# Kernel tuning notes

Hardware: AMD Instinct MI355X
Metric: run time of the kernel (lower is better)

The kernel has to match this reference:

```python
import jax, jax.numpy as jnp
import numpy as np

B, S, D, F, H = 32768, 3, 512, 512, 8
DH = F // H
NEG = 1e9


def setup_inputs() -> dict:
    key = jax.random.key(0)
    ks = jax.random.split(key, 13)
    mk = lambda i, shape: jax.random.normal(ks[i], shape, dtype=jnp.float32)
    return {
        "q": mk(0, (B, S, D)),
        "k": mk(1, (B, S, D)),
        "v": mk(2, (B, S, D)),
        "mask": jax.random.randint(ks[3], (B, S), 0, 2, dtype=jnp.int32),
        "Wq": mk(4, (D, F)) * 0.02, "bq": jnp.zeros((F,), jnp.float32),
        "Wk": mk(5, (D, F)) * 0.02, "bk": jnp.zeros((F,), jnp.float32),
        "Wv": mk(6, (D, F)) * 0.02, "bv": jnp.zeros((F,), jnp.float32),
        "Wo": mk(7, (F, F)) * 0.02, "bo": jnp.zeros((F,), jnp.float32),
    }


def _split_heads(x):
    # [B, S, F] -> [B, H, S, DH]
    b, s, _ = x.shape
    return x.reshape(b, s, H, DH).transpose(0, 2, 1, 3)


def reference(q, k, v, mask, Wq, bq, Wk, bk, Wv, bv, Wo, bo):
    qh = _split_heads(q @ Wq + bq)
    kh = _split_heads(k @ Wk + bk)
    vh = _split_heads(v @ Wv + bv)
    scores = jnp.einsum("bhqd,bhkd->bhqk", qh, kh) / np.sqrt(DH).astype(np.float32)
    m = mask.astype(scores.dtype) * NEG  # [B, S]
    scores = scores - m[:, None, None, :] - m[:, None, :, None]  # col + row mask
    w = jax.nn.softmax(scores, axis=-1)
    attn = jnp.einsum("bhqk,bhkd->bhqd", w, vh)  # [B, H, S, DH]
    attn = attn.transpose(0, 2, 1, 3).reshape(attn.shape[0], S, F)
    return attn @ Wo + bo
```

## Files before the change

### kernel.cpp

```cpp
#include <hip/hip_runtime.h>


typedef __bf16 bf16x8 __attribute__((ext_vector_type(8)));
typedef float f32x4 __attribute__((ext_vector_type(4)));

union U8 { bf16x8 v; unsigned short u[8]; unsigned int w[4]; uint4 q; };

__device__ __forceinline__ unsigned short f2bf(float f) {
  union { float f; unsigned int u; } v; v.f = f;
  unsigned int u = v.u;
  return (unsigned short)((u + 0x7FFFu + ((u >> 16) & 1u)) >> 16);
}
__device__ __forceinline__ unsigned int cvt_pk_bf16(float lo, float hi) {
  unsigned int r;
  asm volatile("v_cvt_pk_bf16_f32 %0, %1, %2" : "=v"(r) : "v"(lo), "v"(hi));
  return r;
}

__global__ void __launch_bounds__(256) wtrans(const float* __restrict__ W0,
                                              const float* __restrict__ W1,
                                              const float* __restrict__ W2,
                                              const float* __restrict__ W3,
                                              unsigned short* __restrict__ out) {
  __shared__ float tile[64][65];
  const float* W = (blockIdx.z == 0) ? W0 : (blockIdx.z == 1) ? W1
                   : (blockIdx.z == 2) ? W2 : W3;
  unsigned short* O = out + (size_t)blockIdx.z * 512 * 512;
  int t = threadIdx.x;
  int k0 = blockIdx.x * 64, n0 = blockIdx.y * 64;
#pragma unroll
  for (int i = 0; i < 4; ++i) {
    int r = (t >> 4) + i * 16;
    int c = (t & 15) * 4;
    float4 v = *(const float4*)(W + (k0 + r) * 512 + n0 + c);
    tile[r][c] = v.x; tile[r][c + 1] = v.y; tile[r][c + 2] = v.z; tile[r][c + 3] = v.w;
  }
  __syncthreads();
  int lane = t & 63, f = t >> 6;
  int lr = lane & 15, hi = lane >> 4;
#pragma unroll
  for (int i = 0; i < 2; ++i) {
    int g = f + i * 4;
    int n16l = g & 3, ksl = g >> 2;
    U8 pk;
#pragma unroll
    for (int e = 0; e < 8; ++e)
      pk.u[e] = f2bf(tile[ksl * 32 + hi * 8 + e][n16l * 16 + lr]);
    int n16 = (n0 >> 4) + n16l;
    int ksg = (k0 >> 5) + ksl;
    *(uint4*)(O + (((n16 * 16 + ksg) * 64 + lane) * 8)) = pk.q;
  }
}

#define SH_SCR  49152
#define SH_PS   65536
#define SH_MSK  71680
#define SH_BIAS 71872

__device__ __forceinline__ void stage48(const float* __restrict__ src, int row0,
                                        int t, char* smem) {
#pragma unroll 1
  for (int c = 0; c < 3; ++c) {
    float4 vals[4];
#pragma unroll
    for (int j = 0; j < 4; ++j) {
      int idx = t + (c * 4 + j) * 512;
      int row = idx >> 7, c4 = idx & 127;
      vals[j] = *(const float4*)(src + (size_t)(row0 + row) * 512 + c4 * 4);
    }
#pragma unroll
    for (int j = 0; j < 4; ++j) {
      int idx = t + (c * 4 + j) * 512;
      int row = idx >> 7, c4 = idx & 127;
      uint2 pk;
      pk.x = cvt_pk_bf16(vals[j].x, vals[j].y);
      pk.y = cvt_pk_bf16(vals[j].z, vals[j].w);
      *(uint2*)(smem + ((row * 1024 + c4 * 8) ^ ((row & 7) << 4))) = pk;
    }
  }
}

__device__ __forceinline__ void gemm_proj(const char* smem,
                                          const unsigned short* __restrict__ Bt,
                                          int w, int l, int lr, int lk8,
                                          f32x4 acc[3][4]) {
#pragma unroll 1
  for (int ks = 0; ks < 16; ++ks) {
    int kb = ks * 32 + lk8;
    bf16x8 a[3];
#pragma unroll
    for (int mt = 0; mt < 3; ++mt) {
      int row = mt * 16 + lr;
      a[mt] = *(const bf16x8*)(smem + ((row * 1024 + kb * 2) ^ ((row & 7) << 4)));
    }
#pragma unroll
    for (int np = 0; np < 2; ++np) {
      bf16x8 b[2];
#pragma unroll
      for (int j = 0; j < 2; ++j)
        b[j] = *(const bf16x8*)(Bt + (((w * 4 + np * 2 + j) * 16 + ks) * 64 + l) * 8);
#pragma unroll
      for (int j = 0; j < 2; ++j)
#pragma unroll
        for (int mt = 0; mt < 3; ++mt)
          acc[mt][np * 2 + j] =
              __builtin_amdgcn_mfma_f32_16x16x32_bf16(a[mt], b[j], acc[mt][np * 2 + j], 0, 0, 0);
    }
  }
}

__device__ __forceinline__ void tile_to_afrags(char* scr, const float* biasT, int bofs,
                                               const f32x4 acc[4], float scale,
                                               int lr, int hi, bf16x8* out) {
#pragma unroll
  for (int nt = 0; nt < 4; ++nt) {
    float bv = biasT[bofs + nt * 16];
#pragma unroll
    for (int r = 0; r < 4; ++r) {
      int row = 4 * hi + r;
      int col = nt * 16 + lr;
      int addr = (row * 128 + col * 2) ^ ((row & 7) << 4);
      *(unsigned short*)(scr + addr) = f2bf((acc[nt][r] + bv) * scale);
    }
  }
  asm volatile("s_waitcnt lgkmcnt(0)" ::: "memory");
#pragma unroll
  for (int kb = 0; kb < 2; ++kb) {
    int addr = (lr * 128 + (kb * 32 + hi * 8) * 2) ^ ((lr & 7) << 4);
    out[kb] = *(const bf16x8*)(scr + addr);
  }
  asm volatile("s_waitcnt lgkmcnt(0)" ::: "memory");
}

__global__ void __launch_bounds__(512, 4) fused_attn(
    const float* __restrict__ q, const float* __restrict__ kin, const float* __restrict__ vin,
    const int* __restrict__ mask, const unsigned short* __restrict__ wt,
    const float* __restrict__ bq, const float* __restrict__ bk,
    const float* __restrict__ bv, const float* __restrict__ bo,
    float* __restrict__ out) {
  __shared__ alignas(16) char smem[80064];
  const int t = threadIdx.x;
  const int w = t >> 6;
  const int l = t & 63;
  const int lr = l & 15;
  const int hi = l >> 4;
  const int lk8 = hi * 8;
  const int row0 = blockIdx.x * 48;
  const int batch0 = blockIdx.x * 16;
  char* scr = smem + SH_SCR + w * 2048;
  float* pscr = (float*)(smem + SH_PS + w * 768);
  int* maskb = (int*)(smem + SH_MSK);
  float* biasT = (float*)(smem + SH_BIAS);
  const int bidx = w * 64 + lr;

  if (t < 48) maskb[t] = mask[batch0 * 3 + t];
  biasT[0 * 512 + t] = bq[t];
  biasT[1 * 512 + t] = bk[t];
  biasT[2 * 512 + t] = bv[t];
  biasT[3 * 512 + t] = bo[t];

  const unsigned short* Wtq = wt;
  const unsigned short* Wtk = wt + 512 * 512;
  const unsigned short* Wtv = wt + 2 * 512 * 512;
  const unsigned short* Wto = wt + 3 * 512 * 512;

  stage48(q, row0, t, smem);
  __syncthreads();
  bf16x8 qa[3][2];
  {
    f32x4 aq[3][4] = {};
    gemm_proj(smem, Wtq, w, l, lr, lk8, aq);
#pragma unroll
    for (int mt = 0; mt < 3; ++mt)
      tile_to_afrags(scr, biasT, 0 * 512 + bidx, aq[mt], 0.125f, lr, hi, qa[mt]);
  }
  __syncthreads();

  stage48(kin, row0, t, smem);
  __syncthreads();
  {
    f32x4 ack[3][4] = {};
    gemm_proj(smem, Wtk, w, l, lr, lk8, ack);

    bf16x8 kf[3][2];
#pragma unroll
    for (int km = 0; km < 3; ++km)
      tile_to_afrags(scr, biasT, 1 * 512 + bidx, ack[km], 1.0f, lr, hi, kf[km]);

#pragma unroll
    for (int km = 0; km < 3; ++km) {
      f32x4 s[3] = {};
#pragma unroll
      for (int qm = 0; qm < 3; ++qm) {
        s[qm] = __builtin_amdgcn_mfma_f32_16x16x32_bf16(qa[qm][0], kf[km][0], s[qm], 0, 0, 0);
        s[qm] = __builtin_amdgcn_mfma_f32_16x16x32_bf16(qa[qm][1], kf[km][1], s[qm], 0, 0, 0);
      }
#pragma unroll
      for (int qm = 0; qm < 3; ++qm)
#pragma unroll
        for (int r = 0; r < 4; ++r) {
          int qrow = qm * 16 + hi * 4 + r;
          int krow = km * 16 + lr;
          int qb = qrow / 3, kb2 = krow / 3;
          if (qb == kb2) pscr[qrow * 4 + (krow - kb2 * 3)] = s[qm][r];
        }
    }
    asm volatile("s_waitcnt lgkmcnt(0)" ::: "memory");
#pragma unroll
    for (int mt = 0; mt < 3; ++mt) {
      int row = mt * 16 + lr;
      int b = row / 3;
      int qi = row - b * 3;
      float s0 = pscr[row * 4 + 0], s1 = pscr[row * 4 + 1], s2 = pscr[row * 4 + 2];
      float m0 = (float)maskb[b * 3 + 0] * 1e9f;
      float m1 = (float)maskb[b * 3 + 1] * 1e9f;
      float m2 = (float)maskb[b * 3 + 2] * 1e9f;
      float mq = (qi == 0) ? m0 : (qi == 1) ? m1 : m2;
      float t0 = (s0 - m0) - mq;
      float t1 = (s1 - m1) - mq;
      float t2 = (s2 - m2) - mq;
      float mx = fmaxf(fmaxf(t0, t1), t2);
      float e0 = __expf(t0 - mx), e1 = __expf(t1 - mx), e2 = __expf(t2 - mx);
      float inv = 1.0f / (e0 + e1 + e2);
      asm volatile("s_waitcnt lgkmcnt(0)" ::: "memory");
      pscr[row * 4 + 0] = e0 * inv;
      pscr[row * 4 + 1] = e1 * inv;
      pscr[row * 4 + 2] = e2 * inv;
    }
  }
  __syncthreads();

  stage48(vin, row0, t, smem);
  __syncthreads();
  f32x4 acv[3][4] = {};
  gemm_proj(smem, Wtv, w, l, lr, lk8, acv);

  bf16x8 pa[3][2];
#pragma unroll
  for (int mt = 0; mt < 3; ++mt) {
    int row = mt * 16 + lr;
    int b3 = (row / 3) * 3;
    float pr0 = pscr[row * 4 + 0];
    float pr1 = pscr[row * 4 + 1];
    float pr2 = pscr[row * 4 + 2];
#pragma unroll
    for (int kb = 0; kb < 2; ++kb) {
      U8 f;
#pragma unroll
      for (int e = 0; e < 8; ++e) {
        int k = kb * 32 + lk8 + e;
        int j = k - b3;
        float pv_ = (j == 0) ? pr0 : (j == 1) ? pr1 : (j == 2) ? pr2 : 0.f;
        f.u[e] = f2bf(pv_);
      }
      pa[mt][kb] = f.v;
    }
  }

  __syncthreads();

#pragma unroll
  for (int nt = 0; nt < 4; ++nt) {
    float bvl = biasT[2 * 512 + bidx + nt * 16];
#pragma unroll
    for (int mt = 0; mt < 3; ++mt)
#pragma unroll
      for (int r = 0; r < 4; ++r) {
        int k = mt * 16 + hi * 4 + r;
        *(unsigned short*)(scr + k * 40 + lr * 2) = f2bf(acv[mt][nt][r] + bvl);
      }
    asm volatile("s_waitcnt lgkmcnt(0)" ::: "memory");
    bf16x8 vb[2];
#pragma unroll
    for (int kb = 0; kb < 2; ++kb) {
      int base = (kb == 0) ? (8 * hi) * 40 : ((hi < 2) ? (32 + 8 * hi) * 40 : 0);
      U8 f;
#pragma unroll
      for (int e = 0; e < 8; ++e)
        f.u[e] = *(const unsigned short*)(scr + base + e * 40 + lr * 2);
      vb[kb] = f.v;
    }
    asm volatile("s_waitcnt lgkmcnt(0)" ::: "memory");
#pragma unroll
    for (int mt = 0; mt < 3; ++mt) {
      f32x4 po = {};
      po = __builtin_amdgcn_mfma_f32_16x16x32_bf16(pa[mt][0], vb[0], po, 0, 0, 0);
      po = __builtin_amdgcn_mfma_f32_16x16x32_bf16(pa[mt][1], vb[1], po, 0, 0, 0);
#pragma unroll
      for (int r = 0; r < 4; ++r) {
        int row = mt * 16 + hi * 4 + r;
        int col = w * 64 + nt * 16 + lr;
        *(unsigned short*)(smem + ((row * 1024 + col * 2) ^ ((row & 7) << 4))) =
            f2bf(po[r]);
      }
    }
  }
  __syncthreads();

  f32x4 ao[3][4] = {};
  gemm_proj(smem, Wto, w, l, lr, lk8, ao);
#pragma unroll
  for (int mt = 0; mt < 3; ++mt)
#pragma unroll
    for (int nt = 0; nt < 4; ++nt) {
      float bvo = biasT[3 * 512 + bidx + nt * 16];
#pragma unroll
      for (int r = 0; r < 4; ++r) {
        int grow = row0 + mt * 16 + hi * 4 + r;
        int col = w * 64 + nt * 16 + lr;
        out[(size_t)grow * 512 + col] = ao[mt][nt][r] + bvo;
      }
    }
}

extern "C" void kernel_launch(void* const* d_in, const int* in_sizes, int n_in,
                              void* d_out, int out_size, void* d_ws, size_t ws_size,
                              hipStream_t stream) {
  const float* q = (const float*)d_in[0];
  const float* k = (const float*)d_in[1];
  const float* v = (const float*)d_in[2];
  const int* mask = (const int*)d_in[3];
  const float* Wq = (const float*)d_in[4];
  const float* bq = (const float*)d_in[5];
  const float* Wk = (const float*)d_in[6];
  const float* bk = (const float*)d_in[7];
  const float* Wv = (const float*)d_in[8];
  const float* bv = (const float*)d_in[9];
  const float* Wo = (const float*)d_in[10];
  const float* bo = (const float*)d_in[11];
  float* out = (float*)d_out;
  unsigned short* wt = (unsigned short*)d_ws;

  wtrans<<<dim3(8, 8, 4), 256, 0, stream>>>(Wq, Wk, Wv, Wo, wt);
  fused_attn<<<2048, 512, 0, stream>>>(q, k, v, mask, wt, bq, bk, bv, bo, out);
}
```

Before: 376.8 us.

## Double wavefronts per block and prefetch next input while projecting

Doubles the block to 16 waves, each owning half a head (32 columns), so the per-head QK dot product is split across wave pairs and summed through shared memory before the softmax. The global loads for the next input (k, then v) are issued into registers before the current projection GEMM and written to LDS afterwards, so HBM latency overlaps with MFMA work. Plain syncthreads calls are replaced with explicit barrier helpers. In exchange it uses more LDS and more registers per block, which may limit residency at 1024 threads per block.

```diff
diff --git a/kernel.cpp b/kernel.cpp
--- a/kernel.cpp
+++ b/kernel.cpp
@@ -15,6 +15,13 @@
   unsigned int r;
   asm volatile("v_cvt_pk_bf16_f32 %0, %1, %2" : "=v"(r) : "v"(lo), "v"(hi));
   return r;
+}
+
+__device__ __forceinline__ void block_sync() {
+  __builtin_amdgcn_sched_barrier(0);
+  asm volatile("s_waitcnt lgkmcnt(0)" ::: "memory");
+  __builtin_amdgcn_s_barrier();
+  __builtin_amdgcn_sched_barrier(0);
 }
 
 __global__ void __launch_bounds__(256) wtrans(const float* __restrict__ W0,
@@ -53,37 +60,36 @@
 }
 
 #define SH_SCR  49152
-#define SH_PS   65536
-#define SH_MSK  71680
-#define SH_BIAS 71872
-
-__device__ __forceinline__ void stage48(const float* __restrict__ src, int row0,
-                                        int t, char* smem) {
-#pragma unroll 1
-  for (int c = 0; c < 3; ++c) {
-    float4 vals[4];
-#pragma unroll
-    for (int j = 0; j < 4; ++j) {
-      int idx = t + (c * 4 + j) * 512;
-      int row = idx >> 7, c4 = idx & 127;
-      vals[j] = *(const float4*)(src + (size_t)(row0 + row) * 512 + c4 * 4);
-    }
-#pragma unroll
-    for (int j = 0; j < 4; ++j) {
-      int idx = t + (c * 4 + j) * 512;
-      int row = idx >> 7, c4 = idx & 127;
-      uint2 pk;
-      pk.x = cvt_pk_bf16(vals[j].x, vals[j].y);
-      pk.y = cvt_pk_bf16(vals[j].z, vals[j].w);
-      *(uint2*)(smem + ((row * 1024 + c4 * 8) ^ ((row & 7) << 4))) = pk;
-    }
+#define SH_PS   81920
+#define SH_MSK  94208
+#define SH_BIAS 94400
+
+__device__ __forceinline__ void stage_issue(const float* __restrict__ src, int row0,
+                                            int t, float4* pre) {
+#pragma unroll
+  for (int i = 0; i < 6; ++i) {
+    int idx = t + i * 1024;
+    int row = idx >> 7, c4 = idx & 127;
+    pre[i] = *(const float4*)(src + (size_t)(row0 + row) * 512 + c4 * 4);
+  }
+  __builtin_amdgcn_sched_barrier(0);
+}
+__device__ __forceinline__ void stage_write(char* smem, int t, const float4* pre) {
+#pragma unroll
+  for (int i = 0; i < 6; ++i) {
+    int idx = t + i * 1024;
+    int row = idx >> 7, c4 = idx & 127;
+    uint2 pk;
+    pk.x = cvt_pk_bf16(pre[i].x, pre[i].y);
+    pk.y = cvt_pk_bf16(pre[i].z, pre[i].w);
+    *(uint2*)(smem + ((row * 1024 + c4 * 8) ^ ((row & 7) << 4))) = pk;
   }
 }
 
 __device__ __forceinline__ void gemm_proj(const char* smem,
                                           const unsigned short* __restrict__ Bt,
-                                          int w, int l, int lr, int lk8,
-                                          f32x4 acc[3][4]) {
+                                          int wn2, int l, int lr, int lk8,
+                                          f32x4 acc[3][2]) {
 #pragma unroll 1
   for (int ks = 0; ks < 16; ++ks) {
     int kb = ks * 32 + lk8;
@@ -93,108 +99,109 @@
       int row = mt * 16 + lr;
       a[mt] = *(const bf16x8*)(smem + ((row * 1024 + kb * 2) ^ ((row & 7) << 4)));
     }
-#pragma unroll
-    for (int np = 0; np < 2; ++np) {
-      bf16x8 b[2];
-#pragma unroll
-      for (int j = 0; j < 2; ++j)
-        b[j] = *(const bf16x8*)(Bt + (((w * 4 + np * 2 + j) * 16 + ks) * 64 + l) * 8);
-#pragma unroll
-      for (int j = 0; j < 2; ++j)
-#pragma unroll
-        for (int mt = 0; mt < 3; ++mt)
-          acc[mt][np * 2 + j] =
-              __builtin_amdgcn_mfma_f32_16x16x32_bf16(a[mt], b[j], acc[mt][np * 2 + j], 0, 0, 0);
-    }
-  }
-}
-
-__device__ __forceinline__ void tile_to_afrags(char* scr, const float* biasT, int bofs,
-                                               const f32x4 acc[4], float scale,
-                                               int lr, int hi, bf16x8* out) {
-#pragma unroll
-  for (int nt = 0; nt < 4; ++nt) {
+    bf16x8 b[2];
+#pragma unroll
+    for (int nt = 0; nt < 2; ++nt)
+      b[nt] = *(const bf16x8*)(Bt + (((wn2 + nt) * 16 + ks) * 64 + l) * 8);
+#pragma unroll
+    for (int nt = 0; nt < 2; ++nt)
+#pragma unroll
+      for (int mt = 0; mt < 3; ++mt)
+        acc[mt][nt] =
+            __builtin_amdgcn_mfma_f32_16x16x32_bf16(a[mt], b[nt], acc[mt][nt], 0, 0, 0);
+  }
+}
+
+__device__ __forceinline__ void tile_to_afrag(char* scr, const float* biasT, int bofs,
+                                              const f32x4 acc[2], float scale,
+                                              int lr, int hi, bf16x8* out1) {
+#pragma unroll
+  for (int nt = 0; nt < 2; ++nt) {
     float bv = biasT[bofs + nt * 16];
 #pragma unroll
     for (int r = 0; r < 4; ++r) {
       int row = 4 * hi + r;
       int col = nt * 16 + lr;
-      int addr = (row * 128 + col * 2) ^ ((row & 7) << 4);
-      *(unsigned short*)(scr + addr) = f2bf((acc[nt][r] + bv) * scale);
+      *(unsigned short*)(scr + row * 72 + col * 2) = f2bf((acc[nt][r] + bv) * scale);
     }
   }
   asm volatile("s_waitcnt lgkmcnt(0)" ::: "memory");
-#pragma unroll
-  for (int kb = 0; kb < 2; ++kb) {
-    int addr = (lr * 128 + (kb * 32 + hi * 8) * 2) ^ ((lr & 7) << 4);
-    out[kb] = *(const bf16x8*)(scr + addr);
-  }
+  *out1 = *(const bf16x8*)(scr + lr * 72 + hi * 16);
   asm volatile("s_waitcnt lgkmcnt(0)" ::: "memory");
 }
 
-__global__ void __launch_bounds__(512, 4) fused_attn(
+__global__ void __launch_bounds__(1024, 4) fused_attn(
     const float* __restrict__ q, const float* __restrict__ kin, const float* __restrict__ vin,
     const int* __restrict__ mask, const unsigned short* __restrict__ wt,
     const float* __restrict__ bq, const float* __restrict__ bk,
     const float* __restrict__ bv, const float* __restrict__ bo,
     float* __restrict__ out) {
-  __shared__ alignas(16) char smem[80064];
+  __shared__ alignas(16) char smem[102592];
   const int t = threadIdx.x;
   const int w = t >> 6;
   const int l = t & 63;
   const int lr = l & 15;
   const int hi = l >> 4;
   const int lk8 = hi * 8;
+  const int h = w >> 1;
+  const int hf = w & 1;
+  const int wn2 = h * 4 + hf * 2;
+  const int colbase = h * 64 + hf * 32;
   const int row0 = blockIdx.x * 48;
   const int batch0 = blockIdx.x * 16;
   char* scr = smem + SH_SCR + w * 2048;
-  float* pscr = (float*)(smem + SH_PS + w * 768);
+  float* pscrW = (float*)(smem + SH_PS + w * 768);
+  float* pscrP = (float*)(smem + SH_PS + (w ^ 1) * 768);
   int* maskb = (int*)(smem + SH_MSK);
   float* biasT = (float*)(smem + SH_BIAS);
-  const int bidx = w * 64 + lr;
+  const int bidx = colbase + lr;
 
   if (t < 48) maskb[t] = mask[batch0 * 3 + t];
-  biasT[0 * 512 + t] = bq[t];
-  biasT[1 * 512 + t] = bk[t];
-  biasT[2 * 512 + t] = bv[t];
-  biasT[3 * 512 + t] = bo[t];
+  if (t < 512) {
+    biasT[0 * 512 + t] = bq[t];
+    biasT[1 * 512 + t] = bk[t];
+    biasT[2 * 512 + t] = bv[t];
+    biasT[3 * 512 + t] = bo[t];
+  }
 
   const unsigned short* Wtq = wt;
   const unsigned short* Wtk = wt + 512 * 512;
   const unsigned short* Wtv = wt + 2 * 512 * 512;
   const unsigned short* Wto = wt + 3 * 512 * 512;
 
-  stage48(q, row0, t, smem);
+  float4 pre[6];
+
+  stage_issue(q, row0, t, pre);
+  stage_write(smem, t, pre);
   __syncthreads();
-  bf16x8 qa[3][2];
+
+  stage_issue(kin, row0, t, pre);
+  bf16x8 qa[3];
   {
-    f32x4 aq[3][4] = {};
-    gemm_proj(smem, Wtq, w, l, lr, lk8, aq);
+    f32x4 aq[3][2] = {};
+    gemm_proj(smem, Wtq, wn2, l, lr, lk8, aq);
 #pragma unroll
     for (int mt = 0; mt < 3; ++mt)
-      tile_to_afrags(scr, biasT, 0 * 512 + bidx, aq[mt], 0.125f, lr, hi, qa[mt]);
-  }
-  __syncthreads();
-
-  stage48(kin, row0, t, smem);
-  __syncthreads();
+      tile_to_afrag(scr, biasT, 0 * 512 + bidx, aq[mt], 0.125f, lr, hi, &qa[mt]);
+  }
+  block_sync();
+  stage_write(smem, t, pre);
+  block_sync();
+
+  stage_issue(vin, row0, t, pre);
   {
-    f32x4 ack[3][4] = {};
-    gemm_proj(smem, Wtk, w, l, lr, lk8, ack);
-
-    bf16x8 kf[3][2];
+    f32x4 ack[3][2] = {};
+    gemm_proj(smem, Wtk, wn2, l, lr, lk8, ack);
+    bf16x8 kf[3];
 #pragma unroll
     for (int km = 0; km < 3; ++km)
-      tile_to_afrags(scr, biasT, 1 * 512 + bidx, ack[km], 1.0f, lr, hi, kf[km]);
-
+      tile_to_afrag(scr, biasT, 1 * 512 + bidx, ack[km], 1.0f, lr, hi, &kf[km]);
 #pragma unroll
     for (int km = 0; km < 3; ++km) {
       f32x4 s[3] = {};
 #pragma unroll
-      for (int qm = 0; qm < 3; ++qm) {
-        s[qm] = __builtin_amdgcn_mfma_f32_16x16x32_bf16(qa[qm][0], kf[km][0], s[qm], 0, 0, 0);
-        s[qm] = __builtin_amdgcn_mfma_f32_16x16x32_bf16(qa[qm][1], kf[km][1], s[qm], 0, 0, 0);
-      }
+      for (int qm = 0; qm < 3; ++qm)
+        s[qm] = __builtin_amdgcn_mfma_f32_16x16x32_bf16(qa[qm], kf[km], s[qm], 0, 0, 0);
 #pragma unroll
       for (int qm = 0; qm < 3; ++qm)
 #pragma unroll
@@ -202,47 +209,44 @@
           int qrow = qm * 16 + hi * 4 + r;
           int krow = km * 16 + lr;
           int qb = qrow / 3, kb2 = krow / 3;
-          if (qb == kb2) pscr[qrow * 4 + (krow - kb2 * 3)] = s[qm][r];
+          if (qb == kb2) pscrW[qrow * 4 + (krow - kb2 * 3)] = s[qm][r];
         }
     }
-    asm volatile("s_waitcnt lgkmcnt(0)" ::: "memory");
-#pragma unroll
-    for (int mt = 0; mt < 3; ++mt) {
-      int row = mt * 16 + lr;
-      int b = row / 3;
-      int qi = row - b * 3;
-      float s0 = pscr[row * 4 + 0], s1 = pscr[row * 4 + 1], s2 = pscr[row * 4 + 2];
-      float m0 = (float)maskb[b * 3 + 0] * 1e9f;
-      float m1 = (float)maskb[b * 3 + 1] * 1e9f;
-      float m2 = (float)maskb[b * 3 + 2] * 1e9f;
-      float mq = (qi == 0) ? m0 : (qi == 1) ? m1 : m2;
-      float t0 = (s0 - m0) - mq;
-      float t1 = (s1 - m1) - mq;
-      float t2 = (s2 - m2) - mq;
-      float mx = fmaxf(fmaxf(t0, t1), t2);
-      float e0 = __expf(t0 - mx), e1 = __expf(t1 - mx), e2 = __expf(t2 - mx);
-      float inv = 1.0f / (e0 + e1 + e2);
-      asm volatile("s_waitcnt lgkmcnt(0)" ::: "memory");
-      pscr[row * 4 + 0] = e0 * inv;
-      pscr[row * 4 + 1] = e1 * inv;
-      pscr[row * 4 + 2] = e2 * inv;
-    }
-  }
-  __syncthreads();
-
-  stage48(vin, row0, t, smem);
-  __syncthreads();
-  f32x4 acv[3][4] = {};
-  gemm_proj(smem, Wtv, w, l, lr, lk8, acv);
+  }
+  block_sync();
+  stage_write(smem, t, pre);
+
+  float p[3][3];
+#pragma unroll
+  for (int mt = 0; mt < 3; ++mt) {
+    int row = mt * 16 + lr;
+    int b = row / 3;
+    int qi = row - b * 3;
+    float s0 = pscrW[row * 4 + 0] + pscrP[row * 4 + 0];
+    float s1 = pscrW[row * 4 + 1] + pscrP[row * 4 + 1];
+    float s2 = pscrW[row * 4 + 2] + pscrP[row * 4 + 2];
+    float m0 = (float)maskb[b * 3 + 0] * 1e9f;
+    float m1 = (float)maskb[b * 3 + 1] * 1e9f;
+    float m2 = (float)maskb[b * 3 + 2] * 1e9f;
+    float mq = (qi == 0) ? m0 : (qi == 1) ? m1 : m2;
+    float t0 = (s0 - m0) - mq;
+    float t1 = (s1 - m1) - mq;
+    float t2 = (s2 - m2) - mq;
+    float mx = fmaxf(fmaxf(t0, t1), t2);
+    float e0 = __expf(t0 - mx), e1 = __expf(t1 - mx), e2 = __expf(t2 - mx);
+    float inv = 1.0f / (e0 + e1 + e2);
+    p[mt][0] = e0 * inv; p[mt][1] = e1 * inv; p[mt][2] = e2 * inv;
+  }
+  block_sync();
+
+  f32x4 acv[3][2] = {};
+  gemm_proj(smem, Wtv, wn2, l, lr, lk8, acv);
 
   bf16x8 pa[3][2];
 #pragma unroll
   for (int mt = 0; mt < 3; ++mt) {
     int row = mt * 16 + lr;
     int b3 = (row / 3) * 3;
-    float pr0 = pscr[row * 4 + 0];
-    float pr1 = pscr[row * 4 + 1];
-    float pr2 = pscr[row * 4 + 2];
 #pragma unroll
     for (int kb = 0; kb < 2; ++kb) {
       U8 f;
@@ -250,17 +254,16 @@
       for (int e = 0; e < 8; ++e) {
         int k = kb * 32 + lk8 + e;
         int j = k - b3;
-        float pv_ = (j == 0) ? pr0 : (j == 1) ? pr1 : (j == 2) ? pr2 : 0.f;
+        float pv_ = (j == 0) ? p[mt][0] : (j == 1) ? p[mt][1] : (j == 2) ? p[mt][2] : 0.f;
         f.u[e] = f2bf(pv_);
       }
       pa[mt][kb] = f.v;
     }
   }
-
-  __syncthreads();
-
-#pragma unroll
-  for (int nt = 0; nt < 4; ++nt) {
+  block_sync();
+
+#pragma unroll
+  for (int nt = 0; nt < 2; ++nt) {
     float bvl = biasT[2 * 512 + bidx + nt * 16];
 #pragma unroll
     for (int mt = 0; mt < 3; ++mt)
@@ -289,25 +292,25 @@
 #pragma unroll
       for (int r = 0; r < 4; ++r) {
         int row = mt * 16 + hi * 4 + r;
-        int col = w * 64 + nt * 16 + lr;
+        int col = colbase + nt * 16 + lr;
         *(unsigned short*)(smem + ((row * 1024 + col * 2) ^ ((row & 7) << 4))) =
             f2bf(po[r]);
       }
     }
   }
-  __syncthreads();
-
-  f32x4 ao[3][4] = {};
-  gemm_proj(smem, Wto, w, l, lr, lk8, ao);
+  block_sync();
+
+  f32x4 ao[3][2] = {};
+  gemm_proj(smem, Wto, wn2, l, lr, lk8, ao);
 #pragma unroll
   for (int mt = 0; mt < 3; ++mt)
 #pragma unroll
-    for (int nt = 0; nt < 4; ++nt) {
+    for (int nt = 0; nt < 2; ++nt) {
       float bvo = biasT[3 * 512 + bidx + nt * 16];
 #pragma unroll
       for (int r = 0; r < 4; ++r) {
         int grow = row0 + mt * 16 + hi * 4 + r;
-        int col = w * 64 + nt * 16 + lr;
+        int col = colbase + nt * 16 + lr;
         out[(size_t)grow * 512 + col] = ao[mt][nt][r] + bvo;
       }
     }
@@ -332,5 +335,5 @@
   unsigned short* wt = (unsigned short*)d_ws;
 
   wtrans<<<dim3(8, 8, 4), 256, 0, stream>>>(Wq, Wk, Wv, Wo, wt);
-  fused_attn<<<2048, 512, 0, stream>>>(q, k, v, mask, wt, bq, bk, bv, bo, out);
-}
+  fused_attn<<<2048, 1024, 0, stream>>>(q, k, v, mask, wt, bq, bk, bv, bo, out);
+}
```

New measurement: 496.0 us. +31.6%, slower.
